# Optimization experiments

Hardware: AMD Instinct MI355X
Metric: run time of the kernel (lower is better)

The kernel has to match this reference:

```python
import jax, jax.numpy as jnp
import numpy as np


def setup_inputs() -> dict:
    key = jax.random.key(0)
    B, S, N, H, GS = 2, 4096, 16, 64, 128
    k0, k1, k2, k3, k4 = jax.random.split(key, 5)
    # per-modality [start, end) segment boundaries (3 modalities)
    modal_index = np.array([[0, 1024], [1024, 3072], [3072, 4096]], dtype=np.int64)
    return {
        "modal_index": modal_index,
        "query_layer": jax.random.normal(k0, (B, S, N, H), jnp.float32),
        "key_layer": jax.random.normal(k1, (B, S, N, H), jnp.float32),
        "value_layer": jax.random.normal(k2, (B, S, N, H), jnp.float32),
        "local_attention_mask": jnp.zeros((B, 1, 1, S), jnp.float32),
        "global_attention_mask_is_not_None": 1,
        "global_k": jax.random.normal(k3, (B, N, GS, H), jnp.float32),
        "global_v": jax.random.normal(k4, (B, N, GS, H), jnp.float32),
        "global_selection_padding_mask_zeros": jnp.zeros((B, 1, 1, GS), jnp.float32),
    }


def reference(modal_index, query_layer, key_layer, value_layer,
              local_attention_mask, global_attention_mask_is_not_None,
              global_k, global_v, global_selection_padding_mask_zeros):
    # [B,S,N,H] -> [B,N,S,H] (matches permute(0,2,1,3) in the torch module)
    q = jnp.transpose(query_layer, (0, 2, 1, 3))
    k = jnp.transpose(key_layer, (0, 2, 1, 3))
    v = jnp.transpose(value_layer, (0, 2, 1, 3))
    H = q.shape[-1]
    gs = global_k.shape[2]
    scale = 1.0 / jnp.sqrt(jnp.asarray(H, q.dtype))
    segments = [(int(a), int(b)) for a, b in np.asarray(modal_index)]

    outs = []
    for st, en in segments:  # small fixed modality count, not a data-dim loop
        qs = q[:, :, st:en]            # [B,N,s,H]
        ks = k[:, :, st:en]
        vs = v[:, :, st:en]
        # local scores within the segment + additive local key mask slice
        scores_l = jnp.einsum('bnqh,bnkh->bnqk', qs, ks) * scale \
                   + local_attention_mask[:, :, :, st:en]        # [B,N,s,s]
        if global_attention_mask_is_not_None:
            scores_g = jnp.einsum('bnqh,bngh->bnqg', qs, global_k) * scale \
                       + global_selection_padding_mask_zeros      # [B,N,s,gs]
            probs = jax.nn.softmax(jnp.concatenate([scores_g, scores_l], axis=-1), axis=-1)
            ctx = jnp.einsum('bnqg,bngh->bnqh', probs[..., :gs], global_v) \
                  + jnp.einsum('bnqk,bnkh->bnqh', probs[..., gs:], vs)
        else:
            ctx = jnp.einsum('bnqk,bnkh->bnqh', jax.nn.softmax(scores_l, axis=-1), vs)
        outs.append(ctx)

    out = jnp.concatenate(outs, axis=2)           # [B,N,S,H]
    return jnp.transpose(out, (0, 2, 1, 3))       # back to [B,S,N,H]
```

## Files before the change

### kernel.cpp

```cpp
#include <hip/hip_runtime.h>

typedef unsigned int u32;
typedef unsigned short u16;
typedef __attribute__((ext_vector_type(8))) short bf16x8;
typedef __attribute__((ext_vector_type(4))) float f32x4;

#define BB 2
#define SS 4096
#define NN 16
#define HH 64
#define GSZ 128
#define QT 64
#define KT 64
#define KP 72
#define VP 72
#define PP 72
#define SCALE 0.125f

__device__ __forceinline__ u16 f2bf(float f){
    u32 x = __float_as_uint(f);
    return (u16)((x + 0x7fffu + ((x >> 16) & 1u)) >> 16);
}
__device__ __forceinline__ u32 pk2(float a, float b){
    return (u32)f2bf(a) | ((u32)f2bf(b) << 16);
}

__global__ __launch_bounds__(256, 2) void mmattn_mfma(
    const void* __restrict__ modal_index, int nseg,
    const float* __restrict__ Q, const float* __restrict__ K, const float* __restrict__ V,
    const float* __restrict__ LM, const int* __restrict__ hasg_p,
    const float* __restrict__ GK, const float* __restrict__ GV, const float* __restrict__ GM,
    float* __restrict__ Out)
{
    __shared__ u16 Klds[KT * KP];
    __shared__ u16 Vt  [HH * VP];
    __shared__ u16 Pl  [4 * 16 * PP];

    const int b = blockIdx.z, n = blockIdx.y;
    const int q0 = blockIdx.x * QT;
    const int tid  = threadIdx.x;
    const int wid  = tid >> 6, lane = tid & 63;
    const int lr   = lane & 15, lg = lane >> 4;

    const int*       p32 = (const int*)modal_index;
    const long long* p64 = (const long long*)modal_index;
    const bool is32 = (p32[2 * nseg - 1] == SS);
    int st = 0, en = SS;
    for (int i = 0; i < nseg; ++i) {
        int a = is32 ? p32[2*i]   : (int)p64[2*i];
        int c = is32 ? p32[2*i+1] : (int)p64[2*i+1];
        if (q0 >= a && q0 < c) { st = a; en = c; }
    }

    bf16x8 qa0, qa1;
    {
        const float* qp = Q + (((size_t)(b * SS + q0 + wid * 16 + lr)) * NN + n) * HH + lg * 8;
        float4 f0 = *(const float4*)(qp);
        float4 f1 = *(const float4*)(qp + 4);
        float4 f2 = *(const float4*)(qp + 32);
        float4 f3 = *(const float4*)(qp + 36);
        union { u32 w[4]; bf16x8 v; } ua, ub;
        ua.w[0]=pk2(f0.x,f0.y); ua.w[1]=pk2(f0.z,f0.w); ua.w[2]=pk2(f1.x,f1.y); ua.w[3]=pk2(f1.z,f1.w);
        ub.w[0]=pk2(f2.x,f2.y); ub.w[1]=pk2(f2.z,f2.w); ub.w[2]=pk2(f3.x,f3.y); ub.w[3]=pk2(f3.z,f3.w);
        qa0 = ua.v; qa1 = ub.v;
    }

    f32x4 o[4];
    #pragma unroll
    for (int hb = 0; hb < 4; ++hb) { o[hb][0]=0.f; o[hb][1]=0.f; o[hb][2]=0.f; o[hb][3]=0.f; }
    float m[4] = {-1e30f,-1e30f,-1e30f,-1e30f};
    float l[4] = {0.f,0.f,0.f,0.f};

    const int sr  = tid >> 2;
    const int scq = tid & 3;

    auto tile = [&](const float* kb_, const float* vb_, size_t rs, const float* mp) {
        {
            const float* kp = kb_ + (size_t)sr * rs + scq * 16;
            float4 k0 = *(const float4*)(kp);
            float4 k1 = *(const float4*)(kp + 4);
            float4 k2 = *(const float4*)(kp + 8);
            float4 k3 = *(const float4*)(kp + 12);
            uint4* kd = (uint4*)&Klds[sr * KP + scq * 16];
            kd[0] = make_uint4(pk2(k0.x,k0.y), pk2(k0.z,k0.w), pk2(k1.x,k1.y), pk2(k1.z,k1.w));
            kd[1] = make_uint4(pk2(k2.x,k2.y), pk2(k2.z,k2.w), pk2(k3.x,k3.y), pk2(k3.z,k3.w));

            const float* vp = vb_ + (size_t)sr * rs + scq * 16;
            float4 v0 = *(const float4*)(vp);
            float4 v1 = *(const float4*)(vp + 4);
            float4 v2 = *(const float4*)(vp + 8);
            float4 v3 = *(const float4*)(vp + 12);
            float vv[16] = {v0.x,v0.y,v0.z,v0.w, v1.x,v1.y,v1.z,v1.w,
                            v2.x,v2.y,v2.z,v2.w, v3.x,v3.y,v3.z,v3.w};
            #pragma unroll
            for (int j = 0; j < 16; ++j)
                Vt[(scq * 16 + j) * VP + sr] = f2bf(vv[j]);
        }
        __syncthreads();

        float mk[4];
        #pragma unroll
        for (int cb = 0; cb < 4; ++cb) mk[cb] = mp[cb * 16 + lr];

        f32x4 s[4];
        #pragma unroll
        for (int cb = 0; cb < 4; ++cb) {
            const bf16x8 kb0 = *(const bf16x8*)&Klds[(cb*16 + lr) * KP + lg*8];
            const bf16x8 kb1 = *(const bf16x8*)&Klds[(cb*16 + lr) * KP + 32 + lg*8];
            f32x4 acc; acc[0]=0.f; acc[1]=0.f; acc[2]=0.f; acc[3]=0.f;
            acc = __builtin_amdgcn_mfma_f32_16x16x32_bf16(qa0, kb0, acc, 0, 0, 0);
            acc = __builtin_amdgcn_mfma_f32_16x16x32_bf16(qa1, kb1, acc, 0, 0, 0);
            s[cb] = acc;
        }

        float cr[4];
        #pragma unroll
        for (int r = 0; r < 4; ++r) {
            float s0 = s[0][r]*SCALE + mk[0];
            float s1 = s[1][r]*SCALE + mk[1];
            float s2 = s[2][r]*SCALE + mk[2];
            float s3 = s[3][r]*SCALE + mk[3];
            float mx = fmaxf(fmaxf(s0, s1), fmaxf(s2, s3));
            mx = fmaxf(mx, __shfl_xor(mx, 1));
            mx = fmaxf(mx, __shfl_xor(mx, 2));
            mx = fmaxf(mx, __shfl_xor(mx, 4));
            mx = fmaxf(mx, __shfl_xor(mx, 8));
            float nm = fmaxf(m[r], mx);
            float c_ = __expf(m[r] - nm);
            m[r] = nm;
            float p0 = __expf(s0 - nm), p1 = __expf(s1 - nm);
            float p2 = __expf(s2 - nm), p3 = __expf(s3 - nm);
            float rsum = ((p0 + p1) + (p2 + p3));
            rsum += __shfl_xor(rsum, 1);
            rsum += __shfl_xor(rsum, 2);
            rsum += __shfl_xor(rsum, 4);
            rsum += __shfl_xor(rsum, 8);
            l[r] = l[r] * c_ + rsum;
            cr[r] = c_;
            u16* pw = &Pl[wid * 16 * PP + (lg * 4 + r) * PP + lr];
            pw[0]  = f2bf(p0); pw[16] = f2bf(p1);
            pw[32] = f2bf(p2); pw[48] = f2bf(p3);
        }
        #pragma unroll
        for (int hb = 0; hb < 4; ++hb) {
            o[hb][0]*=cr[0]; o[hb][1]*=cr[1]; o[hb][2]*=cr[2]; o[hb][3]*=cr[3];
        }

        const bf16x8 pa0 = *(const bf16x8*)&Pl[wid*16*PP + lr*PP + lg*8];
        const bf16x8 pa1 = *(const bf16x8*)&Pl[wid*16*PP + lr*PP + 32 + lg*8];
        #pragma unroll
        for (int hb = 0; hb < 4; ++hb) {
            const bf16x8 vb0 = *(const bf16x8*)&Vt[(hb*16 + lr) * VP + lg*8];
            const bf16x8 vb1 = *(const bf16x8*)&Vt[(hb*16 + lr) * VP + 32 + lg*8];
            o[hb] = __builtin_amdgcn_mfma_f32_16x16x32_bf16(pa0, vb0, o[hb], 0, 0, 0);
            o[hb] = __builtin_amdgcn_mfma_f32_16x16x32_bf16(pa1, vb1, o[hb], 0, 0, 0);
        }
        __syncthreads();
    };

    if (*hasg_p) {
        const float* gkb = GK + ((size_t)(b * NN + n)) * GSZ * HH;
        const float* gvb = GV + ((size_t)(b * NN + n)) * GSZ * HH;
        const float* gmb = GM + (size_t)b * GSZ;
        tile(gkb,            gvb,            HH, gmb);
        tile(gkb + 64 * HH,  gvb + 64 * HH,  HH, gmb + 64);
    }
    {
        const float* lmb = LM + (size_t)b * SS;
        for (int k0 = st; k0 < en; k0 += KT) {
            const float* kb_ = K + (((size_t)(b * SS + k0)) * NN + n) * HH;
            const float* vb_ = V + (((size_t)(b * SS + k0)) * NN + n) * HH;
            tile(kb_, vb_, (size_t)NN * HH, lmb + k0);
        }
    }

    float inv[4] = {1.f/l[0], 1.f/l[1], 1.f/l[2], 1.f/l[3]};
    #pragma unroll
    for (int hb = 0; hb < 4; ++hb) {
        #pragma unroll
        for (int r = 0; r < 4; ++r) {
            const int qrow = q0 + wid * 16 + lg * 4 + r;
            Out[(((size_t)(b * SS + qrow)) * NN + n) * HH + hb * 16 + lr] = o[hb][r] * inv[r];
        }
    }
}

extern "C" void kernel_launch(void* const* d_in, const int* in_sizes, int n_in,
                              void* d_out, int out_size, void* d_ws, size_t ws_size,
                              hipStream_t stream)
{
    const void* modal = d_in[0];
    const int   nseg  = in_sizes[0] / 2;
    const float* Q  = (const float*)d_in[1];
    const float* K  = (const float*)d_in[2];
    const float* V  = (const float*)d_in[3];
    const float* LM = (const float*)d_in[4];
    const int*   HG = (const int*)d_in[5];
    const float* GK = (const float*)d_in[6];
    const float* GV = (const float*)d_in[7];
    const float* GM = (const float*)d_in[8];
    float* Out = (float*)d_out;

    dim3 grid(SS / QT, NN, BB);
    mmattn_mfma<<<grid, dim3(256), 0, stream>>>(modal, nseg, Q, K, V, LM, HG, GK, GV, GM, Out);
}
```

Before: 394.0 us.

## Pre-convert K/V to bf16 in workspace, double query tile, remap blocks per XCD

Adds a prep kernel that converts K, V, global K and global V to bf16 once in the workspace. The attention kernel then loads half as many bytes per tile and skips the repeated per-block fp32-to-bf16 conversion. The query tile grows to 128 rows with 512 threads (8 waves), so each K/V tile staged in shared memory is reused by twice as many queries. Blocks are remapped so that each XCD handles contiguous (batch, head) pairs for L2 locality, and the LDS pitch changes to 70. The cost is an extra kernel launch plus a full pass over K/V, and a larger block that may reduce occupancy.

```diff
diff --git a/kernel.cpp b/kernel.cpp
--- a/kernel.cpp
+++ b/kernel.cpp
@@ -10,11 +10,9 @@
 #define NN 16
 #define HH 64
 #define GSZ 128
-#define QT 64
+#define QT 128
 #define KT 64
-#define KP 72
-#define VP 72
-#define PP 72
+#define PITCH 70
 #define SCALE 0.125f
 
 __device__ __forceinline__ u16 f2bf(float f){
@@ -25,22 +23,48 @@
     return (u32)f2bf(a) | ((u32)f2bf(b) << 16);
 }
 
-__global__ __launch_bounds__(256, 2) void mmattn_mfma(
+__global__ __launch_bounds__(256) void prep_bf16(
+    const float* __restrict__ K, const float* __restrict__ V,
+    const float* __restrict__ GK, const float* __restrict__ GV,
+    u16* __restrict__ ws, size_t NK, size_t NG)
+{
+    size_t idx = ((size_t)blockIdx.x * 256 + threadIdx.x) * 8;
+    const float* src;
+    if      (idx < NK)          src = K  + idx;
+    else if (idx < 2*NK)        src = V  + (idx - NK);
+    else if (idx < 2*NK + NG)   src = GK + (idx - 2*NK);
+    else                        src = GV + (idx - 2*NK - NG);
+    float4 a = *(const float4*)src;
+    float4 b = *(const float4*)(src + 4);
+    uint4 o = make_uint4(pk2(a.x,a.y), pk2(a.z,a.w), pk2(b.x,b.y), pk2(b.z,b.w));
+    *(uint4*)(ws + idx) = o;
+}
+
+template<int PRE>
+__global__ __launch_bounds__(512, 4) void mmattn_mfma(
     const void* __restrict__ modal_index, int nseg,
-    const float* __restrict__ Q, const float* __restrict__ K, const float* __restrict__ V,
+    const float* __restrict__ Q,  const float* __restrict__ Kf, const float* __restrict__ Vf,
     const float* __restrict__ LM, const int* __restrict__ hasg_p,
-    const float* __restrict__ GK, const float* __restrict__ GV, const float* __restrict__ GM,
+    const float* __restrict__ GKf, const float* __restrict__ GVf, const float* __restrict__ GM,
+    const u16* __restrict__ Kb, const u16* __restrict__ Vb,
+    const u16* __restrict__ GKb, const u16* __restrict__ GVb,
     float* __restrict__ Out)
 {
-    __shared__ u16 Klds[KT * KP];
-    __shared__ u16 Vt  [HH * VP];
-    __shared__ u16 Pl  [4 * 16 * PP];
-
-    const int b = blockIdx.z, n = blockIdx.y;
-    const int q0 = blockIdx.x * QT;
-    const int tid  = threadIdx.x;
-    const int wid  = tid >> 6, lane = tid & 63;
-    const int lr   = lane & 15, lg = lane >> 4;
+    __shared__ u16 Klds[KT * PITCH];
+    __shared__ u16 Vt  [HH * PITCH];
+    __shared__ u16 Pl  [8 * 16 * PITCH];
+
+    const int bid = blockIdx.x;
+    const int xcd = bid & 7, ii = bid >> 3;
+    const int p   = xcd * 4 + (ii >> 5);
+    const int b   = p >> 4, n = p & 15;
+    const int q0  = (ii & 31) * QT;
+
+    const int tid = threadIdx.x;
+    const int wid = tid >> 6, lane = tid & 63;
+    const int lr  = lane & 15, lg = lane >> 4;
+    const int srow = tid >> 3;
+    const int sc8  = (tid & 7) * 8;
 
     const int*       p32 = (const int*)modal_index;
     const long long* p64 = (const long long*)modal_index;
@@ -71,30 +95,30 @@
     float m[4] = {-1e30f,-1e30f,-1e30f,-1e30f};
     float l[4] = {0.f,0.f,0.f,0.f};
 
-    const int sr  = tid >> 2;
-    const int scq = tid & 3;
-
-    auto tile = [&](const float* kb_, const float* vb_, size_t rs, const float* mp) {
-        {
-            const float* kp = kb_ + (size_t)sr * rs + scq * 16;
-            float4 k0 = *(const float4*)(kp);
-            float4 k1 = *(const float4*)(kp + 4);
-            float4 k2 = *(const float4*)(kp + 8);
-            float4 k3 = *(const float4*)(kp + 12);
-            uint4* kd = (uint4*)&Klds[sr * KP + scq * 16];
-            kd[0] = make_uint4(pk2(k0.x,k0.y), pk2(k0.z,k0.w), pk2(k1.x,k1.y), pk2(k1.z,k1.w));
-            kd[1] = make_uint4(pk2(k2.x,k2.y), pk2(k2.z,k2.w), pk2(k3.x,k3.y), pk2(k3.z,k3.w));
-
-            const float* vp = vb_ + (size_t)sr * rs + scq * 16;
-            float4 v0 = *(const float4*)(vp);
-            float4 v1 = *(const float4*)(vp + 4);
-            float4 v2 = *(const float4*)(vp + 8);
-            float4 v3 = *(const float4*)(vp + 12);
-            float vv[16] = {v0.x,v0.y,v0.z,v0.w, v1.x,v1.y,v1.z,v1.w,
-                            v2.x,v2.y,v2.z,v2.w, v3.x,v3.y,v3.z,v3.w};
+    u16* Plw = &Pl[wid * 16 * PITCH];
+
+    auto tile = [&](const void* kb, const void* vb, size_t rs, const float* mp) {
+        if constexpr (PRE) {
+            const u16* kp = (const u16*)kb + (size_t)srow * rs + sc8;
+            *(uint4*)&Klds[srow * PITCH + sc8] = *(const uint4*)kp;
+            const u16* vp = (const u16*)vb + (size_t)srow * rs + sc8;
+            uint4 w = *(const uint4*)vp;
+            u16 vv[8] = {(u16)w.x,(u16)(w.x>>16),(u16)w.y,(u16)(w.y>>16),
+                         (u16)w.z,(u16)(w.z>>16),(u16)w.w,(u16)(w.w>>16)};
             #pragma unroll
-            for (int j = 0; j < 16; ++j)
-                Vt[(scq * 16 + j) * VP + sr] = f2bf(vv[j]);
+            for (int j = 0; j < 8; ++j) Vt[(sc8 + j) * PITCH + srow] = vv[j];
+        } else {
+            const float* kp = (const float*)kb + (size_t)srow * rs + sc8;
+            float4 ka = *(const float4*)kp;
+            float4 kc = *(const float4*)(kp + 4);
+            *(uint4*)&Klds[srow * PITCH + sc8] =
+                make_uint4(pk2(ka.x,ka.y), pk2(ka.z,ka.w), pk2(kc.x,kc.y), pk2(kc.z,kc.w));
+            const float* vp = (const float*)vb + (size_t)srow * rs + sc8;
+            float4 va = *(const float4*)vp;
+            float4 vc = *(const float4*)(vp + 4);
+            float vv[8] = {va.x,va.y,va.z,va.w, vc.x,vc.y,vc.z,vc.w};
+            #pragma unroll
+            for (int j = 0; j < 8; ++j) Vt[(sc8 + j) * PITCH + srow] = f2bf(vv[j]);
         }
         __syncthreads();
 
@@ -105,8 +129,8 @@
         f32x4 s[4];
         #pragma unroll
         for (int cb = 0; cb < 4; ++cb) {
-            const bf16x8 kb0 = *(const bf16x8*)&Klds[(cb*16 + lr) * KP + lg*8];
-            const bf16x8 kb1 = *(const bf16x8*)&Klds[(cb*16 + lr) * KP + 32 + lg*8];
+            const bf16x8 kb0 = *(const bf16x8*)&Klds[(cb*16 + lr) * PITCH + lg*8];
+            const bf16x8 kb1 = *(const bf16x8*)&Klds[(cb*16 + lr) * PITCH + 32 + lg*8];
             f32x4 acc; acc[0]=0.f; acc[1]=0.f; acc[2]=0.f; acc[3]=0.f;
             acc = __builtin_amdgcn_mfma_f32_16x16x32_bf16(qa0, kb0, acc, 0, 0, 0);
             acc = __builtin_amdgcn_mfma_f32_16x16x32_bf16(qa1, kb1, acc, 0, 0, 0);
@@ -130,14 +154,14 @@
             m[r] = nm;
             float p0 = __expf(s0 - nm), p1 = __expf(s1 - nm);
             float p2 = __expf(s2 - nm), p3 = __expf(s3 - nm);
-            float rsum = ((p0 + p1) + (p2 + p3));
+            float rsum = (p0 + p1) + (p2 + p3);
             rsum += __shfl_xor(rsum, 1);
             rsum += __shfl_xor(rsum, 2);
             rsum += __shfl_xor(rsum, 4);
             rsum += __shfl_xor(rsum, 8);
             l[r] = l[r] * c_ + rsum;
             cr[r] = c_;
-            u16* pw = &Pl[wid * 16 * PP + (lg * 4 + r) * PP + lr];
+            u16* pw = &Plw[(lg * 4 + r) * PITCH + lr];
             pw[0]  = f2bf(p0); pw[16] = f2bf(p1);
             pw[32] = f2bf(p2); pw[48] = f2bf(p3);
         }
@@ -146,12 +170,12 @@
             o[hb][0]*=cr[0]; o[hb][1]*=cr[1]; o[hb][2]*=cr[2]; o[hb][3]*=cr[3];
         }
 
-        const bf16x8 pa0 = *(const bf16x8*)&Pl[wid*16*PP + lr*PP + lg*8];
-        const bf16x8 pa1 = *(const bf16x8*)&Pl[wid*16*PP + lr*PP + 32 + lg*8];
+        const bf16x8 pa0 = *(const bf16x8*)&Plw[lr * PITCH + lg*8];
+        const bf16x8 pa1 = *(const bf16x8*)&Plw[lr * PITCH + 32 + lg*8];
         #pragma unroll
         for (int hb = 0; hb < 4; ++hb) {
-            const bf16x8 vb0 = *(const bf16x8*)&Vt[(hb*16 + lr) * VP + lg*8];
-            const bf16x8 vb1 = *(const bf16x8*)&Vt[(hb*16 + lr) * VP + 32 + lg*8];
+            const bf16x8 vb0 = *(const bf16x8*)&Vt[(hb*16 + lr) * PITCH + lg*8];
+            const bf16x8 vb1 = *(const bf16x8*)&Vt[(hb*16 + lr) * PITCH + 32 + lg*8];
             o[hb] = __builtin_amdgcn_mfma_f32_16x16x32_bf16(pa0, vb0, o[hb], 0, 0, 0);
             o[hb] = __builtin_amdgcn_mfma_f32_16x16x32_bf16(pa1, vb1, o[hb], 0, 0, 0);
         }
@@ -159,18 +183,31 @@
     };
 
     if (*hasg_p) {
-        const float* gkb = GK + ((size_t)(b * NN + n)) * GSZ * HH;
-        const float* gvb = GV + ((size_t)(b * NN + n)) * GSZ * HH;
         const float* gmb = GM + (size_t)b * GSZ;
-        tile(gkb,            gvb,            HH, gmb);
-        tile(gkb + 64 * HH,  gvb + 64 * HH,  HH, gmb + 64);
+        if constexpr (PRE) {
+            const u16* gkb = GKb + ((size_t)(b * NN + n)) * GSZ * HH;
+            const u16* gvb = GVb + ((size_t)(b * NN + n)) * GSZ * HH;
+            tile(gkb,           gvb,           HH, gmb);
+            tile(gkb + 64*HH,   gvb + 64*HH,   HH, gmb + 64);
+        } else {
+            const float* gkb = GKf + ((size_t)(b * NN + n)) * GSZ * HH;
+            const float* gvb = GVf + ((size_t)(b * NN + n)) * GSZ * HH;
+            tile(gkb,           gvb,           HH, gmb);
+            tile(gkb + 64*HH,   gvb + 64*HH,   HH, gmb + 64);
+        }
     }
     {
         const float* lmb = LM + (size_t)b * SS;
         for (int k0 = st; k0 < en; k0 += KT) {
-            const float* kb_ = K + (((size_t)(b * SS + k0)) * NN + n) * HH;
-            const float* vb_ = V + (((size_t)(b * SS + k0)) * NN + n) * HH;
-            tile(kb_, vb_, (size_t)NN * HH, lmb + k0);
+            if constexpr (PRE) {
+                tile(Kb + (((size_t)(b * SS + k0)) * NN + n) * HH,
+                     Vb + (((size_t)(b * SS + k0)) * NN + n) * HH,
+                     (size_t)NN * HH, lmb + k0);
+            } else {
+                tile(Kf + (((size_t)(b * SS + k0)) * NN + n) * HH,
+                     Vf + (((size_t)(b * SS + k0)) * NN + n) * HH,
+                     (size_t)NN * HH, lmb + k0);
+            }
         }
     }
 
@@ -201,6 +238,20 @@
     const float* GM = (const float*)d_in[8];
     float* Out = (float*)d_out;
 
-    dim3 grid(SS / QT, NN, BB);
-    mmattn_mfma<<<grid, dim3(256), 0, stream>>>(modal, nseg, Q, K, V, LM, HG, GK, GV, GM, Out);
-}
+    const size_t NK = (size_t)BB * SS * NN * HH;
+    const size_t NG = (size_t)BB * NN * GSZ * HH;
+    const size_t need = (2*NK + 2*NG) * sizeof(u16);
+
+    const int nblk = (SS / QT) * NN * BB;
+
+    if (d_ws && ws_size >= need) {
+        u16* wsp = (u16*)d_ws;
+        const size_t tot8 = (2*NK + 2*NG) / 8;
+        prep_bf16<<<(int)(tot8 / 256), 256, 0, stream>>>(K, V, GK, GV, wsp, NK, NG);
+        mmattn_mfma<1><<<nblk, 512, 0, stream>>>(modal, nseg, Q, K, V, LM, HG, GK, GV, GM,
+                                                 wsp, wsp + NK, wsp + 2*NK, wsp + 2*NK + NG, Out);
+    } else {
+        mmattn_mfma<0><<<nblk, 512, 0, stream>>>(modal, nseg, Q, K, V, LM, HG, GK, GV, GM,
+                                                 nullptr, nullptr, nullptr, nullptr, Out);
+    }
+}
```

Result: slower. 435.6 us (+10.5%).
